# Kernel optimization log

Hardware: AMD Instinct MI355X
Metric: run time of the kernel (lower is better)

The kernel has to match this reference:

```python
import math
import itertools
import jax, jax.numpy as jnp
import numpy as np

SEQ_LEN = 16
D_IN = 2048
TSS = 3          # temporal_set_size
D_OUT = 1128
PE_SCALE = 0.1
N_SUPPORT = 5
N_QUERIES = 1
LN_EPS = 1e-5


def _pos_enc(seq_len, d_model):
    pos = np.arange(seq_len, dtype=np.float32)[:, None]
    div = np.exp(np.arange(0, d_model, 2, dtype=np.float32) * -(math.log(10000.0) / d_model))
    pe = np.zeros((seq_len, d_model), dtype=np.float32)
    pe[:, 0::2] = np.sin(pos * div) * PE_SCALE
    pe[:, 1::2] = np.cos(pos * div) * PE_SCALE
    return jnp.asarray(pe)


def _tuples(seq_len, k):
    return np.asarray(list(itertools.combinations(range(seq_len), k)), dtype=np.int32)  # [T, k]


def setup_inputs() -> dict:
    key = jax.random.key(0)
    ks = jax.random.split(key, 8)
    return {
        "support_set": jax.random.normal(ks[0], (N_SUPPORT, SEQ_LEN, D_IN), jnp.float32),
        "queries": jax.random.normal(ks[1], (N_QUERIES, SEQ_LEN, D_IN), jnp.float32),
        "support_labels": jnp.arange(N_SUPPORT, dtype=jnp.int64),
        "wk": jax.random.normal(ks[2], (D_OUT, D_IN * TSS), jnp.float32) * 0.02,
        "bk": jax.random.normal(ks[3], (D_OUT,), jnp.float32) * 0.02,
        "wv": jax.random.normal(ks[4], (D_OUT, D_IN * TSS), jnp.float32) * 0.02,
        "bv": jax.random.normal(ks[5], (D_OUT,), jnp.float32) * 0.02,
        "gamma": jnp.ones((D_OUT,), jnp.float32),
        "beta": jnp.zeros((D_OUT,), jnp.float32),
    }


def _layer_norm(x, gamma, beta):
    mu = jnp.mean(x, axis=-1, keepdims=True)
    var = jnp.mean(jnp.square(x - mu), axis=-1, keepdims=True)
    return (x - mu) * jax.lax.rsqrt(var + LN_EPS) * gamma + beta


def reference(support_set, queries, support_labels, wk, bk, wv, bv, gamma, beta):
    tup = _tuples(SEQ_LEN, TSS)                      # [T, 3] static
    T = tup.shape[0]                                 # tuples_len = C(16,3) = 560
    pe = _pos_enc(SEQ_LEN, D_IN)                     # [S, D_IN]

    s = support_set + pe                             # [5, S, D_IN]
    q = queries + pe                                 # [1, S, D_IN]

    # gather frame tuples and flatten: [n, T, 3*D_IN]
    s_t = s[:, tup, :].reshape(N_SUPPORT, T, TSS * D_IN)
    q_t = q[:, tup, :].reshape(N_QUERIES, T, TSS * D_IN)

    s_ks = _layer_norm(s_t @ wk.T + bk, gamma, beta)  # [5, T, D_OUT]
    q_ks = _layer_norm(q_t @ wk.T + bk, gamma, beta)  # [1, T, D_OUT]
    s_vs = s_t @ wv.T + bv                            # [5, T, D_OUT]
    q_vs = q_t @ wv.T + bv                            # [1, T, D_OUT]

    # _extract_class_indices returns the label value itself -> direct row gather
    ck = s_ks[support_labels]                         # [C, T, D_OUT]
    cv = s_vs[support_labels]                         # [C, T, D_OUT]

    scores = jnp.einsum('qtd,csd->cqts', q_ks, ck) / math.sqrt(D_OUT)  # [C, Q, T, T]
    attn = jax.nn.softmax(scores, axis=-1)            # softmax over support tuples
    proto = jnp.einsum('cqts,csd->cqtd', attn, cv)    # [C, Q, T, D_OUT]

    diff = q_vs[None] - proto                         # [C, Q, T, D_OUT]
    dist = -jnp.sum(diff * diff, axis=(-2, -1)) / T   # [C, Q]
    logits = dist.T                                   # [Q, C]
    return logits
```

## Files before the change

kernel.cpp:

```cpp
#include <hip/hip_runtime.h>
#include <hip/hip_bf16.h>

#define SEQ 16
#define DIN 2048
#define TSS 3
#define DOUT 1128
#define DPAD 1152
#define NT 560
#define NTPAD 576
#define NSEQ 6
#define NCOL 6768
#define W1CNT 6930432

typedef __attribute__((ext_vector_type(4))) float f32x4;
typedef __attribute__((ext_vector_type(8))) short bf16x8;

__device__ __forceinline__ float bf2f(unsigned short h) {
    union { unsigned int u; float f; } c; c.u = ((unsigned int)h) << 16; return c.f;
}
__device__ __forceinline__ unsigned short f2bf(float f) {
    union { float f; unsigned int u; } c; c.f = f;
    unsigned int lsb = (c.u >> 16) & 1;
    c.u += 0x7fffu + lsb;
    return (unsigned short)(c.u >> 16);
}
__device__ __forceinline__ float loadf(const void* p, size_t i, int f32m) {
    return f32m ? ((const float*)p)[i] : bf2f(((const unsigned short*)p)[i]);
}
__device__ __forceinline__ int probe_f32(const void* gamma) {
    return (((const unsigned int*)gamma)[0] == 0x3F800000u) ? 1 : 0;
}
__device__ __forceinline__ int probe_i64(const void* labels) {
    return (((const long long*)labels)[1] == 1LL) ? 1 : 0;
}
__device__ __forceinline__ int get_label(const void* p, int c, int is64) {
    long long v = is64 ? ((const long long*)p)[c] : (long long)((const int*)p)[c];
    if (v < 0) v = 0; if (v > 4) v = 4;
    return (int)v;
}


__global__ __launch_bounds__(256) void k_build_wx(
        const void* __restrict__ sup, const void* __restrict__ qry,
        const void* __restrict__ wk, const void* __restrict__ wv,
        const void* __restrict__ gamma,
        unsigned short* __restrict__ X, unsigned short* __restrict__ Wb) {
    int f32m = probe_f32(gamma);
    if (blockIdx.x < 768) {
        int idx = blockIdx.x * 256 + threadIdx.x;
        int d = idx & (DIN - 1);
        int nf = idx >> 11;
        int f = nf & 15, n = nf >> 4;
        float v = (n < 5) ? loadf(sup, (size_t)nf * DIN + d, f32m)
                          : loadf(qry, (size_t)f * DIN + d, f32m);
        int m2 = d & ~1;
        float div = __expf(-(float)m2 * (9.210340371976184f / 2048.0f));
        float ang = (float)f * div;
        float pe = ((d & 1) ? __cosf(ang) : __sinf(ang)) * 0.1f;
        X[idx] = f2bf(v + pe);
    } else {
        size_t t = ((size_t)(blockIdx.x - 768) * 256 + threadIdx.x) * 8;
        int which = t >= (size_t)W1CNT;
        size_t off = t - (which ? (size_t)W1CNT : 0);
        const void* src = which ? wv : wk;
        if (f32m) {
            f32x4 w0 = *(const f32x4*)((const float*)src + off);
            f32x4 w1 = *(const f32x4*)((const float*)src + off + 4);
            bf16x8 o;
#pragma unroll
            for (int j = 0; j < 4; ++j) {
                o[j]     = (short)f2bf(w0[j]);
                o[4 + j] = (short)f2bf(w1[j]);
            }
            *(bf16x8*)(Wb + t) = o;
        } else {
            *(bf16x8*)(Wb + t) = *(const bf16x8*)((const unsigned short*)src + off);
        }
    }
}

__global__ __launch_bounds__(256) void k_proj(
        const unsigned short* __restrict__ X, const unsigned short* __restrict__ Wb,
        unsigned short* __restrict__ Pb) {
    int tn = blockIdx.x;
    int tid = threadIdx.x;
    int w = tid >> 6, lane = tid & 63;
    int c16 = lane & 15, quad = lane >> 4;
    int colA = tn * 32 + c16;
    int colB0 = colA + 16;
    int colB = colB0 > 6767 ? 6767 : colB0;
    int whA = colA / 3384; int reA = colA - whA * 3384;
    int sgA = reA / DOUT;  int oA  = reA - sgA * DOUT;
    int whB = colB / 3384; int reB = colB - whB * 3384;
    int sgB = reB / DOUT;  int oB  = reB - sgB * DOUT;
    const unsigned short* wbA = Wb + (size_t)whA * W1CNT + (size_t)oA * (TSS * DIN) + (size_t)sgA * DIN;
    const unsigned short* wbB = Wb + (size_t)whB * W1CNT + (size_t)oB * (TSS * DIN) + (size_t)sgB * DIN;

    f32x4 acc[6][2];
#pragma unroll
    for (int m = 0; m < 6; ++m)
#pragma unroll
        for (int ch = 0; ch < 2; ++ch) acc[m][ch] = (f32x4){0.f, 0.f, 0.f, 0.f};

    int kb = w * 512;
#pragma unroll 2
    for (int k0 = kb; k0 < kb + 512; k0 += 32) {
        bf16x8 b0 = *(const bf16x8*)(wbA + k0 + quad * 8);
        bf16x8 b1 = *(const bf16x8*)(wbB + k0 + quad * 8);
#pragma unroll
        for (int m = 0; m < 6; ++m) {
            bf16x8 a = *(const bf16x8*)(X + (size_t)(m * 16 + c16) * DIN + k0 + quad * 8);
            acc[m][0] = __builtin_amdgcn_mfma_f32_16x16x32_bf16(a, b0, acc[m][0], 0, 0, 0);
            acc[m][1] = __builtin_amdgcn_mfma_f32_16x16x32_bf16(a, b1, acc[m][1], 0, 0, 0);
        }
    }
    __shared__ float red[3 * 12 * 64 * 4];
    if (w > 0) {
#pragma unroll
        for (int m = 0; m < 6; ++m)
#pragma unroll
            for (int ch = 0; ch < 2; ++ch)
#pragma unroll
                for (int r = 0; r < 4; ++r)
                    red[(((w - 1) * 12 + m * 2 + ch) * 64 + lane) * 4 + r] = acc[m][ch][r];
    }
    __syncthreads();
    if (w == 0) {
#pragma unroll
        for (int m = 0; m < 6; ++m)
#pragma unroll
            for (int ch = 0; ch < 2; ++ch) {
                int t = m * 2 + ch;
#pragma unroll
                for (int r = 0; r < 4; ++r) {
                    float s = acc[m][ch][r]
                            + red[((0 * 12 + t) * 64 + lane) * 4 + r]
                            + red[((1 * 12 + t) * 64 + lane) * 4 + r]
                            + red[((2 * 12 + t) * 64 + lane) * 4 + r];
                    int row = m * 16 + quad * 4 + r;
                    int col = tn * 32 + ch * 16 + c16;
                    if (col < NCOL) Pb[(size_t)row * NCOL + col] = f2bf(s);
                }
            }
    }
}

__global__ __launch_bounds__(256) void k_combine_ln(
        const unsigned short* __restrict__ Pb,
        const void* __restrict__ bk, const void* __restrict__ bv,
        const void* __restrict__ gamma, const void* __restrict__ beta,
        unsigned short* __restrict__ ks, unsigned short* __restrict__ vs) {
    int n = blockIdx.x / NT, t = blockIdx.x % NT;
    int f32m = probe_f32(gamma);
    int idx = t, fi, fj, fk;
    for (fi = 0;; ++fi) { int c2 = (15 - fi) * (14 - fi) / 2; if (idx < c2) break; idx -= c2; }
    for (fj = fi + 1;; ++fj) { int c1 = 15 - fj; if (idx < c1) break; idx -= c1; }
    fk = fj + 1 + idx;
    size_t ri = (size_t)(n * 16 + fi) * NCOL;
    size_t rj = (size_t)(n * 16 + fj) * NCOL;
    size_t rk = (size_t)(n * 16 + fk) * NCOL;

    float kv[5], vv[5];
    float s = 0.f, s2 = 0.f;
#pragma unroll
    for (int it = 0; it < 5; ++it) {
        int o = threadIdx.x + it * 256;
        kv[it] = 0.f; vv[it] = 0.f;
        if (o < DOUT) {
            float a = bf2f(Pb[ri + o]) + bf2f(Pb[rj + DOUT + o])
                    + bf2f(Pb[rk + 2 * DOUT + o]) + loadf(bk, o, f32m);
            float b = bf2f(Pb[ri + 3 * DOUT + o]) + bf2f(Pb[rj + 4 * DOUT + o])
                    + bf2f(Pb[rk + 5 * DOUT + o]) + loadf(bv, o, f32m);
            kv[it] = a; vv[it] = b;
            s += a; s2 += a * a;
        }
    }
    __shared__ float red[8];
#pragma unroll
    for (int off = 32; off; off >>= 1) { s += __shfl_down(s, off); s2 += __shfl_down(s2, off); }
    int wid = threadIdx.x >> 6;
    if ((threadIdx.x & 63) == 0) { red[wid] = s; red[4 + wid] = s2; }
    __syncthreads();
    s = red[0] + red[1] + red[2] + red[3];
    s2 = red[4] + red[5] + red[6] + red[7];
    float mu = s / (float)DOUT;
    float var = s2 / (float)DOUT - mu * mu;
    float rstd = rsqrtf(var + 1e-5f);

    size_t base = ((size_t)n * NT + t) * DPAD;
#pragma unroll
    for (int it = 0; it < 5; ++it) {
        int o = threadIdx.x + it * 256;
        if (o < DOUT) {
            ks[base + o] = f2bf((kv[it] - mu) * rstd * loadf(gamma, o, f32m) + loadf(beta, o, f32m));
            vs[base + o] = f2bf(vv[it]);
        } else if (o < DPAD) {
            ks[base + o] = 0; vs[base + o] = 0;
        }
    }
}

__global__ __launch_bounds__(256) void k_transpose(
        const unsigned short* __restrict__ vs, unsigned short* __restrict__ vsTF) {
    int b = blockIdx.x;
    int tt = b % 18; b /= 18; int ot = b % 36; int n = b / 36;
    int t0 = tt * 32, o0 = ot * 32;
    int tx = threadIdx.x & 31, ty = threadIdx.x >> 5;
    __shared__ unsigned short tile[32][33];
#pragma unroll
    for (int i = 0; i < 4; ++i) {
        int t = t0 + ty + 8 * i;
        tile[ty + 8 * i][tx] = (t < NT) ? vs[((size_t)n * NT + t) * DPAD + o0 + tx] : 0;
    }
    __syncthreads();
#pragma unroll
    for (int i = 0; i < 4; ++i) {
        int r = ty + 8 * i;
        size_t addr = ((size_t)(n * 72 + ot * 2 + (r >> 4)) * 18 + tt) * 512
                    + (size_t)((tx >> 3) * 16 + (r & 15)) * 8 + (tx & 7);
        vsTF[addr] = tile[tx][r];
    }
}

__global__ __launch_bounds__(256) void k_scores(
        const unsigned short* __restrict__ ks, const void* __restrict__ labels,
        float* __restrict__ scores) {
    int b = blockIdx.x;
    int c = b % 5; int rest = b / 5;
    int tm = rest / 9, tn = rest % 9;
    int tid = threadIdx.x;
    int w = tid >> 6, lane = tid & 63;
    int c16 = lane & 15, quad = lane >> 4;
    int lab = get_label(labels, c, probe_i64(labels));
    const unsigned short* arow[4];
    const unsigned short* brow[4];
#pragma unroll
    for (int i = 0; i < 4; ++i) {
        arow[i] = ks + ((size_t)5 * NT + tm * 64 + i * 16 + c16) * DPAD;
        brow[i] = ks + ((size_t)lab * NT + tn * 64 + i * 16 + c16) * DPAD;
    }
    f32x4 acc[4][4];
#pragma unroll
    for (int i = 0; i < 4; ++i)
#pragma unroll
        for (int j = 0; j < 4; ++j) acc[i][j] = (f32x4){0.f, 0.f, 0.f, 0.f};

    int kb = w * 288;
#pragma unroll 2
    for (int k0 = kb; k0 < kb + 288; k0 += 32) {
        bf16x8 a[4], bv4[4];
#pragma unroll
        for (int i = 0; i < 4; ++i) a[i]   = *(const bf16x8*)(arow[i] + k0 + quad * 8);
#pragma unroll
        for (int j = 0; j < 4; ++j) bv4[j] = *(const bf16x8*)(brow[j] + k0 + quad * 8);
#pragma unroll
        for (int i = 0; i < 4; ++i)
#pragma unroll
            for (int j = 0; j < 4; ++j)
                acc[i][j] = __builtin_amdgcn_mfma_f32_16x16x32_bf16(a[i], bv4[j], acc[i][j], 0, 0, 0);
    }
    __shared__ float red[3 * 16 * 64 * 4];
    if (w > 0) {
#pragma unroll
        for (int i = 0; i < 4; ++i)
#pragma unroll
            for (int j = 0; j < 4; ++j)
#pragma unroll
                for (int r = 0; r < 4; ++r)
                    red[(((w - 1) * 16 + i * 4 + j) * 64 + lane) * 4 + r] = acc[i][j][r];
    }
    __syncthreads();
    if (w == 0) {
        const float scale = 0.029774540f;
#pragma unroll
        for (int i = 0; i < 4; ++i)
#pragma unroll
            for (int j = 0; j < 4; ++j) {
                int t = i * 4 + j;
#pragma unroll
                for (int r = 0; r < 4; ++r) {
                    float s = acc[i][j][r]
                            + red[((0 * 16 + t) * 64 + lane) * 4 + r]
                            + red[((1 * 16 + t) * 64 + lane) * 4 + r]
                            + red[((2 * 16 + t) * 64 + lane) * 4 + r];
                    int tq = tm * 64 + i * 16 + quad * 4 + r;
                    int ts = tn * 64 + j * 16 + c16;
                    scores[((size_t)c * NTPAD + tq) * NTPAD + ts] = s * scale;
                }
            }
    }
}

__global__ __launch_bounds__(256) void k_softmax(
        const float* __restrict__ scores, unsigned short* __restrict__ attnF) {
    int row = blockIdx.x * 4 + (threadIdx.x >> 6);
    int lane = threadIdx.x & 63;
    int c = row / NTPAD, tq = row % NTPAD;
    unsigned short* dstc = attnF + ((size_t)(c * 36 + (tq >> 4)) * 18) * 512 + (size_t)(tq & 15) * 8;
    if (tq >= NT) {
#pragma unroll
        for (int i = 0; i < 9; ++i) {
            int ts = lane + i * 64;
            dstc[((ts >> 5) << 9) + ((ts >> 3) & 3) * 128 + (ts & 7)] = 0;
        }
        return;
    }
    const float* src = scores + (size_t)row * NTPAD;
    float vals[9];
    float m = -1e30f;
#pragma unroll
    for (int i = 0; i < 9; ++i) {
        int idx = lane + i * 64;
        vals[i] = (idx < NT) ? src[idx] : -1e30f;
        m = fmaxf(m, vals[i]);
    }
#pragma unroll
    for (int off = 32; off; off >>= 1) m = fmaxf(m, __shfl_xor(m, off));
    float s = 0.f;
#pragma unroll
    for (int i = 0; i < 9; ++i) {
        int idx = lane + i * 64;
        vals[i] = (idx < NT) ? __expf(vals[i] - m) : 0.f;
        s += vals[i];
    }
#pragma unroll
    for (int off = 32; off; off >>= 1) s += __shfl_xor(s, off);
    float inv = 1.f / s;
#pragma unroll
    for (int i = 0; i < 9; ++i) {
        int ts = lane + i * 64;
        dstc[((ts >> 5) << 9) + ((ts >> 3) & 3) * 128 + (ts & 7)] =
            (ts < NT) ? f2bf(vals[i] * inv) : 0;
    }
}

__global__ __launch_bounds__(128) void k_proto_dist(
        const unsigned short* __restrict__ attnF, const unsigned short* __restrict__ vs,
        const unsigned short* __restrict__ vsTF,
        const void* __restrict__ labels, float* __restrict__ parts) {
    int b = blockIdx.x;
    int c = b / 162; int rest = b % 162;
    int tm = rest / 18, tn = rest % 18;
    int tid = threadIdx.x;
    int w = tid >> 6, lane = tid & 63;
    int c16 = lane & 15, quad = lane >> 4;
    int lab = get_label(labels, c, probe_i64(labels));
    const unsigned short* aF = attnF + ((size_t)(c * 36 + tm * 4) * 18) * 512 + lane * 8;
    const unsigned short* bF = vsTF + ((size_t)(lab * 72 + tn * 4) * 18) * 512 + lane * 8;
    f32x4 acc[4][4];
#pragma unroll
    for (int i = 0; i < 4; ++i)
#pragma unroll
        for (int j = 0; j < 4; ++j) acc[i][j] = (f32x4){0.f, 0.f, 0.f, 0.f};

    int ktb = w * 9;
#pragma unroll 2
    for (int kt = ktb; kt < ktb + 9; ++kt) {
        bf16x8 a[4], bv4[4];
#pragma unroll
        for (int i = 0; i < 4; ++i) a[i]   = *(const bf16x8*)(aF + ((size_t)(i * 18 + kt) << 9));
#pragma unroll
        for (int j = 0; j < 4; ++j) bv4[j] = *(const bf16x8*)(bF + ((size_t)(j * 18 + kt) << 9));
#pragma unroll
        for (int i = 0; i < 4; ++i)
#pragma unroll
            for (int j = 0; j < 4; ++j)
                acc[i][j] = __builtin_amdgcn_mfma_f32_16x16x32_bf16(a[i], bv4[j], acc[i][j], 0, 0, 0);
    }
    __shared__ float red[16 * 64 * 4];
    if (w == 1) {
#pragma unroll
        for (int i = 0; i < 4; ++i)
#pragma unroll
            for (int j = 0; j < 4; ++j)
#pragma unroll
                for (int r = 0; r < 4; ++r)
                    red[((i * 4 + j) * 64 + lane) * 4 + r] = acc[i][j][r];
    }
    __syncthreads();
    if (w == 0) {
        const unsigned short* qv = vs + (size_t)5 * NT * DPAD;
        float part = 0.f;
#pragma unroll
        for (int i = 0; i < 4; ++i)
#pragma unroll
            for (int j = 0; j < 4; ++j) {
                int t = i * 4 + j;
#pragma unroll
                for (int r = 0; r < 4; ++r) {
                    float s = acc[i][j][r] + red[(t * 64 + lane) * 4 + r];
                    int tq = tm * 64 + i * 16 + quad * 4 + r;
                    int o  = tn * 64 + j * 16 + c16;
                    if (tq < NT && o < DOUT) {
                        float d = bf2f(qv[(size_t)tq * DPAD + o]) - s;
                        part += d * d;
                    }
                }
            }
#pragma unroll
        for (int off = 32; off; off >>= 1) part += __shfl_down(part, off);
        if (lane == 0) parts[blockIdx.x] = part;
    }
}

__global__ __launch_bounds__(320) void k_final(const float* __restrict__ parts,
                                               const void* __restrict__ gamma,
                                               void* __restrict__ out) {
    int c = threadIdx.x >> 6;
    int lane = threadIdx.x & 63;
    float s = 0.f;
    for (int i = lane; i < 162; i += 64) s += parts[c * 162 + i];
#pragma unroll
    for (int off = 32; off; off >>= 1) s += __shfl_down(s, off);
    if (lane == 0) {
        float v = -s * (1.0f / (float)NT);
        if (probe_f32(gamma)) ((float*)out)[c] = v;
        else ((unsigned short*)out)[c] = f2bf(v);
    }
}

extern "C" void kernel_launch(void* const* d_in, const int* in_sizes, int n_in,
                              void* d_out, int out_size, void* d_ws, size_t ws_size,
                              hipStream_t stream) {
    const void* sup   = d_in[0];
    const void* qry   = d_in[1];
    const void* labs  = d_in[2];
    const void* wk    = d_in[3];
    const void* bk    = d_in[4];
    const void* wv    = d_in[5];
    const void* bv    = d_in[6];
    const void* gamma = d_in[7];
    const void* beta  = d_in[8];

    char* ws = (char*)d_ws;
    unsigned short* X      = (unsigned short*)(ws + 256);
    unsigned short* Pb     = (unsigned short*)(ws + 393472);
    float*          parts  = (float*)(ws + 2992384);
    unsigned short* Wb     = (unsigned short*)(ws + 5604352);
    unsigned short* ks     = (unsigned short*)(ws + 33326080);
    unsigned short* vsb    = (unsigned short*)(ws + 41067520);
    float*          scores = (float*)(ws + 48808960);
    unsigned short* attnF  = (unsigned short*)(ws + 55444480);
    unsigned short* vsTF   = (unsigned short*)(ws + 58762240);

    k_build_wx  <<<7536, 256, 0, stream>>>(sup, qry, wk, wv, gamma, X, Wb);
    k_proj      <<<212, 256, 0, stream>>>(X, Wb, Pb);
    k_combine_ln<<<NSEQ * NT, 256, 0, stream>>>(Pb, bk, bv, gamma, beta, ks, vsb);
    k_transpose <<<5 * 36 * 18, 256, 0, stream>>>(vsb, vsTF);
    k_scores    <<<405, 256, 0, stream>>>(ks, labs, scores);
    k_softmax   <<<720, 256, 0, stream>>>(scores, attnF);
    k_proto_dist<<<810, 128, 0, stream>>>(attnF, vsb, vsTF, labs, parts);
    k_final     <<<1, 320, 0, stream>>>(parts, gamma, d_out);
}
```

Measured before the change: 197.1 us.

## Pre-swizzle X, weights and keys into MFMA fragment layout for coalesced loads

The converted inputs, the weight matrix and the layer-normed keys are now written in a tiled fragment order, 16 rows by 32 k-values per 512-element block. Each lane of a wavefront can then load its bf16x8 operand from one contiguous 1 KB region instead of strided rows. This targets the uncoalesced global loads in the projection and score GEMMs. The cost is strided reads in the weight conversion step and scattered writes of the keys in the layernorm kernel.

```diff
diff --git a/kernel.cpp b/kernel.cpp
--- a/kernel.cpp
+++ b/kernel.cpp
@@ -44,57 +44,70 @@
         const void* __restrict__ sup, const void* __restrict__ qry,
         const void* __restrict__ wk, const void* __restrict__ wv,
         const void* __restrict__ gamma,
-        unsigned short* __restrict__ X, unsigned short* __restrict__ Wb) {
+        unsigned short* __restrict__ XF, unsigned short* __restrict__ WbF) {
     int f32m = probe_f32(gamma);
-    if (blockIdx.x < 768) {
-        int idx = blockIdx.x * 256 + threadIdx.x;
-        int d = idx & (DIN - 1);
-        int nf = idx >> 11;
-        int f = nf & 15, n = nf >> 4;
-        float v = (n < 5) ? loadf(sup, (size_t)nf * DIN + d, f32m)
-                          : loadf(qry, (size_t)f * DIN + d, f32m);
-        int m2 = d & ~1;
-        float div = __expf(-(float)m2 * (9.210340371976184f / 2048.0f));
-        float ang = (float)f * div;
-        float pe = ((d & 1) ? __cosf(ang) : __sinf(ang)) * 0.1f;
-        X[idx] = f2bf(v + pe);
+    if (blockIdx.x < 96) {
+        int c8 = blockIdx.x * 256 + threadIdx.x;
+        int idx512 = c8 >> 6;
+        int rowgrp = idx512 >> 6, kt = idx512 & 63;
+        int sub = c8 & 63;
+        int r15 = sub & 15;
+        int row = rowgrp * 16 + r15;
+        int f = row & 15, n = row >> 4;
+        int k = kt * 32 + (sub >> 4) * 8;
+        bf16x8 ov;
+#pragma unroll
+        for (int j = 0; j < 8; ++j) {
+            int d = k + j;
+            float v = (n < 5) ? loadf(sup, (size_t)row * DIN + d, f32m)
+                              : loadf(qry, (size_t)f * DIN + d, f32m);
+            int m2 = d & ~1;
+            float div = __expf(-(float)m2 * (9.210340371976184f / 2048.0f));
+            float ang = (float)f * div;
+            float pe = ((d & 1) ? __cosf(ang) : __sinf(ang)) * 0.1f;
+            ov[j] = (short)f2bf(v + pe);
+        }
+        *(bf16x8*)(XF + (size_t)c8 * 8) = ov;
     } else {
-        size_t t = ((size_t)(blockIdx.x - 768) * 256 + threadIdx.x) * 8;
-        int which = t >= (size_t)W1CNT;
-        size_t off = t - (which ? (size_t)W1CNT : 0);
+        size_t c8 = (size_t)(blockIdx.x - 96) * 256 + threadIdx.x;
+        size_t idx512 = c8 >> 6;
+        int colgrp = (int)(idx512 >> 6);
+        int kt = (int)(idx512 & 63);
+        int sub = (int)(c8 & 63);
+        int col = colgrp * 16 + (sub & 15);
+        int k = kt * 32 + (sub >> 4) * 8;
+        int which = col / 3384; int rem = col - which * 3384;
+        int seg = rem / DOUT;   int o = rem - seg * DOUT;
         const void* src = which ? wv : wk;
+        size_t si = (size_t)o * (TSS * DIN) + (size_t)seg * DIN + k;
         if (f32m) {
-            f32x4 w0 = *(const f32x4*)((const float*)src + off);
-            f32x4 w1 = *(const f32x4*)((const float*)src + off + 4);
-            bf16x8 o;
+            f32x4 w0 = *(const f32x4*)((const float*)src + si);
+            f32x4 w1 = *(const f32x4*)((const float*)src + si + 4);
+            bf16x8 ov;
 #pragma unroll
             for (int j = 0; j < 4; ++j) {
-                o[j]     = (short)f2bf(w0[j]);
-                o[4 + j] = (short)f2bf(w1[j]);
+                ov[j]     = (short)f2bf(w0[j]);
+                ov[4 + j] = (short)f2bf(w1[j]);
             }
-            *(bf16x8*)(Wb + t) = o;
+            *(bf16x8*)(WbF + c8 * 8) = ov;
         } else {
-            *(bf16x8*)(Wb + t) = *(const bf16x8*)((const unsigned short*)src + off);
+            *(bf16x8*)(WbF + c8 * 8) = *(const bf16x8*)((const unsigned short*)src + si);
         }
     }
 }
 
 __global__ __launch_bounds__(256) void k_proj(
-        const unsigned short* __restrict__ X, const unsigned short* __restrict__ Wb,
+        const unsigned short* __restrict__ XF, const unsigned short* __restrict__ WbF,
         unsigned short* __restrict__ Pb) {
     int tn = blockIdx.x;
     int tid = threadIdx.x;
     int w = tid >> 6, lane = tid & 63;
     int c16 = lane & 15, quad = lane >> 4;
-    int colA = tn * 32 + c16;
-    int colB0 = colA + 16;
-    int colB = colB0 > 6767 ? 6767 : colB0;
-    int whA = colA / 3384; int reA = colA - whA * 3384;
-    int sgA = reA / DOUT;  int oA  = reA - sgA * DOUT;
-    int whB = colB / 3384; int reB = colB - whB * 3384;
-    int sgB = reB / DOUT;  int oB  = reB - sgB * DOUT;
-    const unsigned short* wbA = Wb + (size_t)whA * W1CNT + (size_t)oA * (TSS * DIN) + (size_t)sgA * DIN;
-    const unsigned short* wbB = Wb + (size_t)whB * W1CNT + (size_t)oB * (TSS * DIN) + (size_t)sgB * DIN;
+    int cg0 = tn * 2;
+    int cg1 = (tn * 2 + 1 > 422) ? 422 : tn * 2 + 1;
+    const unsigned short* bF0 = WbF + ((size_t)cg0 << 15) + lane * 8;
+    const unsigned short* bF1 = WbF + ((size_t)cg1 << 15) + lane * 8;
+    const unsigned short* aF  = XF + lane * 8;
 
     f32x4 acc[6][2];
 #pragma unroll
@@ -102,14 +115,14 @@
 #pragma unroll
         for (int ch = 0; ch < 2; ++ch) acc[m][ch] = (f32x4){0.f, 0.f, 0.f, 0.f};
 
-    int kb = w * 512;
+    int ktb = w * 16;
 #pragma unroll 2
-    for (int k0 = kb; k0 < kb + 512; k0 += 32) {
-        bf16x8 b0 = *(const bf16x8*)(wbA + k0 + quad * 8);
-        bf16x8 b1 = *(const bf16x8*)(wbB + k0 + quad * 8);
+    for (int kt = ktb; kt < ktb + 16; ++kt) {
+        bf16x8 b0 = *(const bf16x8*)(bF0 + ((size_t)kt << 9));
+        bf16x8 b1 = *(const bf16x8*)(bF1 + ((size_t)kt << 9));
 #pragma unroll
         for (int m = 0; m < 6; ++m) {
-            bf16x8 a = *(const bf16x8*)(X + (size_t)(m * 16 + c16) * DIN + k0 + quad * 8);
+            bf16x8 a = *(const bf16x8*)(aF + ((size_t)(m * 64 + kt) << 9));
             acc[m][0] = __builtin_amdgcn_mfma_f32_16x16x32_bf16(a, b0, acc[m][0], 0, 0, 0);
             acc[m][1] = __builtin_amdgcn_mfma_f32_16x16x32_bf16(a, b1, acc[m][1], 0, 0, 0);
         }
@@ -149,7 +162,7 @@
         const unsigned short* __restrict__ Pb,
         const void* __restrict__ bk, const void* __restrict__ bv,
         const void* __restrict__ gamma, const void* __restrict__ beta,
-        unsigned short* __restrict__ ks, unsigned short* __restrict__ vs) {
+        unsigned short* __restrict__ ksF, unsigned short* __restrict__ vs) {
     int n = blockIdx.x / NT, t = blockIdx.x % NT;
     int f32m = probe_f32(gamma);
     int idx = t, fi, fj, fk;
@@ -187,15 +200,18 @@
     float var = s2 / (float)DOUT - mu * mu;
     float rstd = rsqrtf(var + 1e-5f);
 
-    size_t base = ((size_t)n * NT + t) * DPAD;
+    size_t ntbase = ((size_t)(n * 36 + (t >> 4)) * 36) * 512 + (size_t)(t & 15) * 8;
+    size_t vbase = ((size_t)n * NT + t) * DPAD;
 #pragma unroll
     for (int it = 0; it < 5; ++it) {
         int o = threadIdx.x + it * 256;
-        if (o < DOUT) {
-            ks[base + o] = f2bf((kv[it] - mu) * rstd * loadf(gamma, o, f32m) + loadf(beta, o, f32m));
-            vs[base + o] = f2bf(vv[it]);
-        } else if (o < DPAD) {
-            ks[base + o] = 0; vs[base + o] = 0;
+        if (o < DPAD) {
+            float kres = 0.f;
+            if (o < DOUT)
+                kres = (kv[it] - mu) * rstd * loadf(gamma, o, f32m) + loadf(beta, o, f32m);
+            ksF[ntbase + ((size_t)(o >> 5) << 9) + (((o >> 3) & 3) << 7) + (o & 7)] =
+                (o < DOUT) ? f2bf(kres) : 0;
+            vs[vbase + o] = (o < DOUT) ? f2bf(vv[it]) : 0;
         }
     }
 }
@@ -223,7 +239,7 @@
 }
 
 __global__ __launch_bounds__(256) void k_scores(
-        const unsigned short* __restrict__ ks, const void* __restrict__ labels,
+        const unsigned short* __restrict__ ksF, const void* __restrict__ labels,
         float* __restrict__ scores) {
     int b = blockIdx.x;
     int c = b % 5; int rest = b / 5;
@@ -232,12 +248,12 @@
     int w = tid >> 6, lane = tid & 63;
     int c16 = lane & 15, quad = lane >> 4;
     int lab = get_label(labels, c, probe_i64(labels));
-    const unsigned short* arow[4];
-    const unsigned short* brow[4];
+    const unsigned short* aF[4];
+    const unsigned short* bF[4];
 #pragma unroll
     for (int i = 0; i < 4; ++i) {
-        arow[i] = ks + ((size_t)5 * NT + tm * 64 + i * 16 + c16) * DPAD;
-        brow[i] = ks + ((size_t)lab * NT + tn * 64 + i * 16 + c16) * DPAD;
+        aF[i] = ksF + (((size_t)(5 * 36 + tm * 4 + i) * 36) << 9) + lane * 8;
+        bF[i] = ksF + (((size_t)(lab * 36 + tn * 4 + i) * 36) << 9) + lane * 8;
     }
     f32x4 acc[4][4];
 #pragma unroll
@@ -245,14 +261,14 @@
 #pragma unroll
         for (int j = 0; j < 4; ++j) acc[i][j] = (f32x4){0.f, 0.f, 0.f, 0.f};
 
-    int kb = w * 288;
+    int ktb = w * 9;
 #pragma unroll 2
-    for (int k0 = kb; k0 < kb + 288; k0 += 32) {
+    for (int kt = ktb; kt < ktb + 9; ++kt) {
         bf16x8 a[4], bv4[4];
 #pragma unroll
-        for (int i = 0; i < 4; ++i) a[i]   = *(const bf16x8*)(arow[i] + k0 + quad * 8);
-#pragma unroll
-        for (int j = 0; j < 4; ++j) bv4[j] = *(const bf16x8*)(brow[j] + k0 + quad * 8);
+        for (int i = 0; i < 4; ++i) a[i]   = *(const bf16x8*)(aF[i] + ((size_t)kt << 9));
+#pragma unroll
+        for (int j = 0; j < 4; ++j) bv4[j] = *(const bf16x8*)(bF[j] + ((size_t)kt << 9));
 #pragma unroll
         for (int i = 0; i < 4; ++i)
 #pragma unroll
@@ -433,21 +449,21 @@
     const void* beta  = d_in[8];
 
     char* ws = (char*)d_ws;
-    unsigned short* X      = (unsigned short*)(ws + 256);
+    unsigned short* XF     = (unsigned short*)(ws + 256);
     unsigned short* Pb     = (unsigned short*)(ws + 393472);
     float*          parts  = (float*)(ws + 2992384);
-    unsigned short* Wb     = (unsigned short*)(ws + 5604352);
-    unsigned short* ks     = (unsigned short*)(ws + 33326080);
-    unsigned short* vsb    = (unsigned short*)(ws + 41067520);
-    float*          scores = (float*)(ws + 48808960);
-    unsigned short* attnF  = (unsigned short*)(ws + 55444480);
-    unsigned short* vsTF   = (unsigned short*)(ws + 58762240);
-
-    k_build_wx  <<<7536, 256, 0, stream>>>(sup, qry, wk, wv, gamma, X, Wb);
-    k_proj      <<<212, 256, 0, stream>>>(X, Wb, Pb);
-    k_combine_ln<<<NSEQ * NT, 256, 0, stream>>>(Pb, bk, bv, gamma, beta, ks, vsb);
+    unsigned short* WbF    = (unsigned short*)(ws + 5604352);
+    unsigned short* ksF    = (unsigned short*)(ws + 33326080);
+    unsigned short* vsb    = (unsigned short*)(ws + 41288704);
+    float*          scores = (float*)(ws + 49030144);
+    unsigned short* attnF  = (unsigned short*)(ws + 55665664);
+    unsigned short* vsTF   = (unsigned short*)(ws + 58983424);
+
+    k_build_wx  <<<96 + 6768, 256, 0, stream>>>(sup, qry, wk, wv, gamma, XF, WbF);
+    k_proj      <<<212, 256, 0, stream>>>(XF, WbF, Pb);
+    k_combine_ln<<<NSEQ * NT, 256, 0, stream>>>(Pb, bk, bv, gamma, beta, ksF, vsb);
     k_transpose <<<5 * 36 * 18, 256, 0, stream>>>(vsb, vsTF);
-    k_scores    <<<405, 256, 0, stream>>>(ks, labs, scores);
+    k_scores    <<<405, 256, 0, stream>>>(ksF, labs, scores);
     k_softmax   <<<720, 256, 0, stream>>>(scores, attnF);
     k_proto_dist<<<810, 128, 0, stream>>>(attnF, vsb, vsTF, labs, parts);
     k_final     <<<1, 320, 0, stream>>>(parts, gamma, d_out);
```

After: 190.8 us. -3.2%, faster.
